# Performance work log

Hardware: AMD Instinct MI355X
Metric: run time of the kernel (lower is better)

## Reference

```python
import jax, jax.numpy as jnp
import numpy as np

N = 25000   # total nodes across the batch of graphs
K = 16      # sample_size_per_layer
H = 128     # encoder_hidden_dim
E = 128     # embedding_size
V = 32000   # vocab size
B = 50      # number of graphs / sql sequences
L = 128     # sql sequence length
NT = 4      # tokens per node name
NLAYERS = 3 # sample_layer_size


def _nrm(k, shape):
    return jax.random.normal(k, shape, dtype=jnp.float32) * 0.05


def setup_inputs() -> dict:
    key = jax.random.key(0)
    ks = iter(jax.random.split(key, 48))
    inp = {}
    inp["embed"] = _nrm(next(ks), (V, E))
    for d in ("seq_f", "seq_b", "node"):
        inp[d + "_Wih"] = _nrm(next(ks), (4 * H, E))
        inp[d + "_Whh"] = _nrm(next(ks), (4 * H, H))
        inp[d + "_b"] = _nrm(next(ks), (4 * H,))
    for d in ("fw", "bw"):
        inp[d + "_att0"] = _nrm(next(ks), (2, H))
        inp[d + "_attr"] = _nrm(next(ks), (NLAYERS - 1, 2, 2 * H))
        inp[d + "_Wg0"] = _nrm(next(ks), (H, H))
        inp[d + "_bg0"] = _nrm(next(ks), (H,))
        inp[d + "_Wgr"] = _nrm(next(ks), (NLAYERS - 1, 2 * H, 2 * H))
        inp[d + "_bgr"] = _nrm(next(ks), (NLAYERS - 1, 2 * H))
        inp[d + "_Wo0"] = _nrm(next(ks), (2, H, H))
        inp[d + "_bo0"] = _nrm(next(ks), (2, H))
        inp[d + "_Wor"] = _nrm(next(ks), (NLAYERS - 1, 2, 2 * H, H))
        inp[d + "_bor"] = _nrm(next(ks), (NLAYERS - 1, 2, H))
    inp["node_features"] = jax.random.randint(next(ks), (N, NT), 0, V)
    inp["fw_adj"] = jax.random.randint(next(ks), (N + 1, K), 0, N + 1)  # index N = zero-pad row
    inp["bw_adj"] = jax.random.randint(next(ks), (N + 1, K), 0, N + 1)
    inp["idx_sql_seqs"] = jax.random.randint(next(ks), (B, L), 0, V)
    lens = jax.random.randint(next(ks), (B,), 16, L + 1)
    inp["sql_seqs_lens"] = lens.at[0].set(L)  # ensure max(lens) == L like pad_packed
    inp["max_len"] = 1000  # nodes per graph (equal-size graphs)
    return inp


def _lstm(x, Wih, Whh, b):
    # x: [B, T, E] -> [B, T, H]; torch LSTM gate order i, f, g, o (bih+bhh folded into b)
    xg = jnp.einsum('bte,ge->btg', x, Wih) + b
    h0 = jnp.zeros((x.shape[0], Whh.shape[1]), x.dtype)
    def step(carry, gt):
        h, c = carry
        g = gt + h @ Whh.T
        i, f, gg, o = jnp.split(g, 4, axis=-1)
        c = jax.nn.sigmoid(f) * c + jax.nn.sigmoid(i) * jnp.tanh(gg)
        h = jax.nn.sigmoid(o) * jnp.tanh(c)
        return (h, c), h
    _, hs = jax.lax.scan(step, (h0, h0), jnp.swapaxes(xg, 0, 1))
    return jnp.swapaxes(hs, 0, 1)


def _gated_attn(self_h, neigh, att, Wg, bg, Wo, bo):
    # additive attention over K sampled neighbors, gated context, concat output (2*H)
    scores = jnp.einsum('nkd,d->nk', neigh, att[1]) + (self_h @ att[0])[:, None]
    a = jax.nn.softmax(scores, axis=-1)
    ctx = jnp.einsum('nk,nkd->nd', a, neigh)
    gate = jax.nn.sigmoid(self_h @ Wg + bg)
    from_self = jax.nn.relu(self_h @ Wo[0] + bo[0])
    from_neigh = jax.nn.relu((gate * ctx) @ Wo[1] + bo[1])
    return jnp.concatenate([from_self, from_neigh], axis=-1)


def reference(embed, seq_f_Wih, seq_f_Whh, seq_f_b, seq_b_Wih, seq_b_Whh, seq_b_b,
              node_Wih, node_Whh, node_b,
              fw_att0, fw_attr, fw_Wg0, fw_bg0, fw_Wgr, fw_bgr, fw_Wo0, fw_bo0, fw_Wor, fw_bor,
              bw_att0, bw_attr, bw_Wg0, bw_bg0, bw_Wgr, bw_bgr, bw_Wo0, bw_bo0, bw_Wor, bw_bor,
              node_features, fw_adj, bw_adj, idx_sql_seqs, sql_seqs_lens, max_len):
    Bq, Lq = idx_sql_seqs.shape
    # --- SQL sequence encoder: bi-LSTM with length-aware reverse (pack/pad semantics) ---
    se = embed[idx_sql_seqs]                              # [B, L, E]
    fwd = _lstm(se, seq_f_Wih, seq_f_Whh, seq_f_b)
    rev_idx = jnp.clip(sql_seqs_lens[:, None] - 1 - jnp.arange(Lq)[None, :], 0, Lq - 1)
    se_rev = jnp.take_along_axis(se, rev_idx[..., None], 1)
    bwd = jnp.take_along_axis(_lstm(se_rev, seq_b_Wih, seq_b_Whh, seq_b_b), rev_idx[..., None], 1)
    valid = (jnp.arange(Lq)[None, :] < sql_seqs_lens[:, None])[..., None]
    seqs_encoding = jnp.concatenate([fwd, bwd], -1) * valid  # padded positions zeroed
    seqs_encoding_mask = (idx_sql_seqs == 0)
    # --- node feature encoder: last hidden of a uni-LSTM over node tokens ---
    node_embedding = _lstm(embed[node_features], node_Wih, node_Whh, node_b)[:, -1, :]  # [N, H]
    fw_nbrs = fw_adj[:-1]  # [N, K]
    bw_nbrs = bw_adj[:-1]
    fw_hidden = node_embedding
    bw_hidden = node_embedding
    for l in range(NLAYERS):
        pad = jnp.zeros((1, fw_hidden.shape[1]), fw_hidden.dtype)
        fn = jnp.concatenate([fw_hidden, pad], 0)[fw_nbrs]  # [N, K, d]
        if l == 0:
            fw_hidden = _gated_attn(fw_hidden, fn, fw_att0, fw_Wg0, fw_bg0, fw_Wo0, fw_bo0)
        else:
            j = l - 1
            fw_hidden = _gated_attn(fw_hidden, fn, fw_attr[j], fw_Wgr[j], fw_bgr[j], fw_Wor[j], fw_bor[j])
        bn_ = jnp.concatenate([bw_hidden, pad], 0)[bw_nbrs]
        if l == 0:
            bw_hidden = _gated_attn(bw_hidden, bn_, bw_att0, bw_Wg0, bw_bg0, bw_Wo0, bw_bo0)
        else:
            j = l - 1
            bw_hidden = _gated_attn(bw_hidden, bn_, bw_attr[j], bw_Wgr[j], bw_bgr[j], bw_Wor[j], bw_bor[j])
    hidden = jax.nn.relu(jnp.concatenate([fw_hidden, bw_hidden], -1))  # [N, 4H]
    graph_hidden = hidden.reshape(hidden.shape[0] // max_len, max_len, hidden.shape[1])
    graph_embedding = graph_hidden.max(axis=1)
    return (graph_hidden, graph_embedding, max_len, seqs_encoding, seqs_encoding_mask)
```

## Files before the change

kernel.cpp:

```cpp
#include <hip/hip_runtime.h>
#include <math.h>

#define NN 25000
#define KNB 16
#define HH 128
#define VV 32000
#define BB 50
#define LL 128
#define NTK 4
#define NGRAPH 25
#define GCH 20

typedef __attribute__((ext_vector_type(8))) short s16x8;
typedef __attribute__((ext_vector_type(4))) float f32x4;
typedef _Float16 h16x2 __attribute__((ext_vector_type(2)));

__device__ __forceinline__ float fexp2(float x) {
#if __has_builtin(__builtin_amdgcn_exp2f)
    return __builtin_amdgcn_exp2f(x);
#else
    return exp2f(x);
#endif
}
__device__ __forceinline__ float frcp(float x) {
#if __has_builtin(__builtin_amdgcn_rcpf)
    return __builtin_amdgcn_rcpf(x);
#else
    return 1.f / x;
#endif
}
__device__ __forceinline__ float fsigm(float x) { return frcp(1.f + fexp2(x * -1.4426950408889634f)); }
__device__ __forceinline__ float ftanh(float x) { return 1.f - 2.f * frcp(1.f + fexp2(x * 2.8853900817779268f)); }

__device__ __forceinline__ unsigned short f2bf(float x) {
    unsigned int u = __float_as_uint(x);
    unsigned int r = (u + 0x7fffu + ((u >> 16) & 1u)) >> 16;
    return (unsigned short)r;
}
__device__ __forceinline__ float bf2f(unsigned int b) {
    return __uint_as_float((b & 0xffffu) << 16);
}

template<int CTRL>
__device__ __forceinline__ float qxor(float x) {
#if __has_builtin(__builtin_amdgcn_mov_dpp)
    return __int_as_float(__builtin_amdgcn_mov_dpp(__float_as_int(x), CTRL, 0xf, 0xf, true));
#else
    int m = (CTRL == 0xB1) ? 1 : (CTRL == 0x4E) ? 2 : 3;
    return __shfl_xor(x, m, 64);
#endif
}

__device__ __forceinline__ float hdot(unsigned int a, unsigned int b, float c) {
#if __has_builtin(__builtin_amdgcn_fdot2)
    return __builtin_amdgcn_fdot2(__builtin_bit_cast(h16x2, a), __builtin_bit_cast(h16x2, b), c, false);
#else
    h16x2 av = __builtin_bit_cast(h16x2, a), bv = __builtin_bit_cast(h16x2, b);
    return c + (float)av[0] * (float)bv[0] + (float)av[1] * (float)bv[1];
#endif
}

__global__ __launch_bounds__(256) void embconv_k(const float* __restrict__ e,
                                                 unsigned short* __restrict__ o)
{
    int i = blockIdx.x * 256 + threadIdx.x;
    if (i < VV * 128) o[i] = f2bf(e[i]);
}

__global__ __launch_bounds__(256) void wprep_k(
    const float* __restrict__ ndWih, const float* __restrict__ ndWhh,
    const float* __restrict__ fWg0, const float* __restrict__ fWgr,
    const float* __restrict__ fWo0, const float* __restrict__ fWor,
    const float* __restrict__ bWg0, const float* __restrict__ bWgr,
    const float* __restrict__ bWo0, const float* __restrict__ bWor,
    const float* __restrict__ sfWih, const float* __restrict__ sbWih,
    const float* __restrict__ sfWhh, const float* __restrict__ sbWhh,
    unsigned short* __restrict__ dst)
{
    int idx = blockIdx.x * 256 + threadIdx.x;
    if (idx >= 1146880) return;
    if (idx >= 884736) {
        int r = idx - 884736;
        int d = r >> 17;
        int o = r & 131071;
        int pairIdx = o >> 1, hf = o & 1;
        int k2 = pairIdx >> 9, n = pairIdx & 511;
        int k = k2 * 2 + hf;
        int unit = n >> 2, gate = n & 3;
        const float* W = d ? sbWhh : sfWhh;
        _Float16 hv = (_Float16)W[(gate * 128 + unit) * 128 + k];
        dst[idx] = __builtin_bit_cast(unsigned short, hv);
        return;
    }
    float val;
    if (idx < 131072) {
        int r = idx >> 8, k = idx & 255;
        int unit = r >> 2, gate = r & 3;
        int srow = (gate << 7) + unit;
        val = (k < 128) ? ndWih[srow * 128 + k] : ndWhh[srow * 128 + (k - 128)];
    } else if (idx < 753664) {
        int r = idx - 131072;
        int dir = r / 311296;
        int o = r % 311296;
        const float* Wg0 = dir ? bWg0 : fWg0;
        const float* Wgr = dir ? bWgr : fWgr;
        const float* Wo0 = dir ? bWo0 : fWo0;
        const float* Wor = dir ? bWor : fWor;
        if (o < 16384) {
            int n = o >> 7, k = o & 127;
            val = Wg0[k * 128 + n];
        } else if (o < 147456) {
            int p = o - 16384;
            int j = p >> 16, q = p & 65535;
            int n = q >> 8, k = q & 255;
            val = Wgr[j * 65536 + k * 256 + n];
        } else if (o < 180224) {
            int p = o - 147456;
            int s = p >> 14, q = p & 16383;
            int n = q >> 7, k = q & 127;
            val = Wo0[s * 16384 + k * 128 + n];
        } else {
            int p = o - 180224;
            int js = p >> 15, q = p & 32767;
            int n = q >> 8, k = q & 255;
            val = Wor[js * 32768 + k * 128 + n];
        }
    } else if (idx < 819200) {
        val = sfWih[idx - 753664];
    } else {
        val = sbWih[idx - 819200];
    }
    dst[idx] = f2bf(val);
}

__global__ __launch_bounds__(256) void tokrev_k(const int* __restrict__ idx,
                                                const int* __restrict__ lens,
                                                int* __restrict__ tokrev)
{
    int t = blockIdx.x * 256 + threadIdx.x;
    if (t >= BB * LL) return;
    int b = t / LL, tt = t % LL;
    int r = lens[b] - 1 - tt;
    r = r < 0 ? 0 : (r > LL - 1 ? LL - 1 : r);
    tokrev[t] = idx[b * LL + r];
}

__global__ __launch_bounds__(256) void hgemm1_k(
    const unsigned short* __restrict__ embedbf,
    const int* __restrict__ gidxA, const int* __restrict__ gidxB,
    const unsigned short* __restrict__ WtA, const unsigned short* __restrict__ WtB,
    const float* __restrict__ biasA, const float* __restrict__ biasB,
    float* __restrict__ outA, float* __restrict__ outB)
{
    __shared__ unsigned short Asm[128 * 64];
    __shared__ unsigned short Bsm[128 * 64];
    const int tid = threadIdx.x;
    const int lane = tid & 63, w = tid >> 6;
    const int wm = w >> 1, wn = w & 1;
    const int lane15 = lane & 15, hi = lane >> 4;
    const int y = blockIdx.y;
    const int* gidx = (y < 4) ? gidxA : gidxB;
    const unsigned short* Wt = (y < 4) ? WtA : WtB;
    const float* bias = (y < 4) ? biasA : biasB;
    float* outp = (y < 4) ? outA : outB;
    const int bm0 = blockIdx.x * 128, bn0 = (y & 3) * 128;
    const int M = BB * LL, K = 128;
    f32x4 acc[4][4];
#pragma unroll
    for (int i = 0; i < 4; ++i)
#pragma unroll
        for (int j = 0; j < 4; ++j) acc[i][j] = (f32x4){0.f, 0.f, 0.f, 0.f};

    for (int kt = 0; kt < K; kt += 64) {
#pragma unroll
        for (int r = 0; r < 4; ++r) {
            int id = tid + r * 256;
            int row = id >> 3, cc = id & 7;
            int m = bm0 + row;
            s16x8 v = {0, 0, 0, 0, 0, 0, 0, 0};
            if (m < M) {
                int g = gidx[m];
                v = *(const s16x8*)(embedbf + (size_t)g * 128 + kt + cc * 8);
            }
            int byt = (cc * 16) ^ ((row & 7) << 4);
            *(s16x8*)((char*)Asm + row * 128 + byt) = v;
        }
#pragma unroll
        for (int r = 0; r < 4; ++r) {
            int id = tid + r * 256;
            int row = id >> 3, cc = id & 7;
            s16x8 v = *(const s16x8*)(Wt + (size_t)(bn0 + row) * K + kt + cc * 8);
            int byt = (cc * 16) ^ ((row & 7) << 4);
            *(s16x8*)((char*)Bsm + row * 128 + byt) = v;
        }
        __syncthreads();
#pragma unroll
        for (int ks = 0; ks < 2; ++ks) {
            s16x8 af[4], bf[4];
#pragma unroll
            for (int mi = 0; mi < 4; ++mi) {
                int row = wm * 64 + mi * 16 + lane15;
                int byt = (ks * 64 + (hi * 16)) ^ ((row & 7) << 4);
                af[mi] = *(const s16x8*)((char*)Asm + row * 128 + byt);
            }
#pragma unroll
            for (int ni = 0; ni < 4; ++ni) {
                int row = wn * 64 + ni * 16 + lane15;
                int byt = (ks * 64 + (hi * 16)) ^ ((row & 7) << 4);
                bf[ni] = *(const s16x8*)((char*)Bsm + row * 128 + byt);
            }
#pragma unroll
            for (int mi = 0; mi < 4; ++mi)
#pragma unroll
                for (int ni = 0; ni < 4; ++ni)
                    acc[mi][ni] = __builtin_amdgcn_mfma_f32_16x16x32_bf16(af[mi], bf[ni], acc[mi][ni], 0, 0, 0);
        }
        __syncthreads();
    }
#pragma unroll
    for (int mi = 0; mi < 4; ++mi) {
#pragma unroll
        for (int ni = 0; ni < 4; ++ni) {
            int n = bn0 + wn * 64 + ni * 16 + lane15;
#pragma unroll
            for (int j = 0; j < 4; ++j) {
                int m = bm0 + wm * 64 + mi * 16 + hi * 4 + j;
                if (m < M) {
                    float v = acc[mi][ni][j] + bias[n];
                    int nn = ((n & 127) << 2) | (n >> 7);
                    outp[(size_t)m * 512 + nn] = v;
                }
            }
        }
    }
}

__global__ __launch_bounds__(512, 4) void node_seq_k(
    const unsigned short* __restrict__ embedbf,
    const int* __restrict__ nodefeat,
    const unsigned short* __restrict__ hrd,
    const unsigned short* __restrict__ nodeW,
    const float* __restrict__ ndb,
    unsigned short* __restrict__ hwr,
    unsigned short* __restrict__ cbuf,
    int step,
    const float* __restrict__ xgf, const float* __restrict__ xgb,
    const unsigned short* __restrict__ wseq,
    const int* __restrict__ lens,
    float* __restrict__ senc,
    unsigned short* __restrict__ hseq, float* __restrict__ cseq)
{
    __shared__ __align__(16) unsigned char smem[32768 + 512];
    const int bid = blockIdx.x;
    const int tid = threadIdx.x;

    if (bid >= 784) {
        int sid = bid - 784;
        int dir = sid >= BB ? 1 : 0;
        int b = dir ? sid - BB : sid;
        int len = lens[b];
        int t0 = step * 32;
        if (t0 >= len) return;
        int t1 = t0 + 32 < len ? t0 + 32 : len;
        const float* xg = (dir ? xgb : xgf) + (size_t)b * LL * 512;
        const unsigned int* wp = (const unsigned int*)(wseq + dir * 131072);
        int q = tid & 3, unit = tid >> 2;
        unsigned int wreg[64];
#pragma unroll
        for (int k2 = 0; k2 < 64; ++k2) wreg[k2] = wp[k2 * 512 + tid];
        unsigned short* hlsq = (unsigned short*)smem;
        float cj = 0.f;
        if (step == 0) {
            if (tid < 128) hlsq[tid] = 0;
        } else {
            if (tid < 128) hlsq[tid] = hseq[sid * 128 + tid];
            if (q == 0) cj = cseq[sid * 128 + unit];
        }
        __syncthreads();
        float xcur = xg[(size_t)t0 * 512 + tid];
        int pb = 0;
        for (int t = t0; t < t1; ++t) {
            float xnext = (t + 1 < t1) ? xg[(size_t)(t + 1) * 512 + tid] : 0.f;
            const uint4* hp = (const uint4*)&hlsq[pb * 128];
            float p0 = 0.f, p1 = 0.f, p2 = 0.f, p3 = 0.f;
#pragma unroll
            for (int i = 0; i < 4; ++i) {
                uint4 h0 = hp[i * 4 + 0], h1 = hp[i * 4 + 1], h2 = hp[i * 4 + 2], h3 = hp[i * 4 + 3];
                const unsigned int* w0 = &wreg[i * 16];
                p0 = hdot(h0.x, w0[0], p0);  p0 = hdot(h0.y, w0[1], p0);
                p0 = hdot(h0.z, w0[2], p0);  p0 = hdot(h0.w, w0[3], p0);
                p1 = hdot(h1.x, w0[4], p1);  p1 = hdot(h1.y, w0[5], p1);
                p1 = hdot(h1.z, w0[6], p1);  p1 = hdot(h1.w, w0[7], p1);
                p2 = hdot(h2.x, w0[8], p2);  p2 = hdot(h2.y, w0[9], p2);
                p2 = hdot(h2.z, w0[10], p2); p2 = hdot(h2.w, w0[11], p2);
                p3 = hdot(h3.x, w0[12], p3); p3 = hdot(h3.y, w0[13], p3);
                p3 = hdot(h3.z, w0[14], p3); p3 = hdot(h3.w, w0[15], p3);
            }
            float accv = xcur + ((p0 + p1) + (p2 + p3));
            float tv = (q == 2) ? ftanh(accv) : fsigm(accv);
            float v1 = __shfl_xor(tv, 1), v2 = __shfl_xor(tv, 2), v3 = __shfl_xor(tv, 3);
            if (q == 0) {
                cj = v1 * cj + tv * v2;
                float hv = v3 * ftanh(cj);
                _Float16 hh = (_Float16)hv;
                hlsq[(pb ^ 1) * 128 + unit] = __builtin_bit_cast(unsigned short, hh);
                int tout = dir ? (len - 1 - t) : t;
                senc[((size_t)b * LL + tout) * 256 + dir * 128 + unit] = hv;
            }
            __syncthreads();
            pb ^= 1;
            xcur = xnext;
        }
        if (q == 0) cseq[sid * 128 + unit] = cj;
        if (tid < 128) hseq[sid * 128 + tid] = hlsq[pb * 128 + tid];
        return;
    }

    unsigned short* Asm = (unsigned short*)smem;
    unsigned short* Bsm = (unsigned short*)(smem + 16384);
    const int lane = tid & 63, w = tid >> 6;
    const int wm = w & 1, wn = w >> 1;
    const int lane15 = lane & 15, hi = lane >> 4, q = lane & 3;
    const int bx = bid % 196, y = bid / 196;
    const int bm0 = bx * 128, bn0 = y * 128;
    const int czero = (step == 0);

    f32x4 acc[4][2];
#pragma unroll
    for (int i = 0; i < 4; ++i)
#pragma unroll
        for (int j = 0; j < 2; ++j) acc[i][j] = (f32x4){0.f, 0.f, 0.f, 0.f};

    for (int kt = 0; kt < 256; kt += 64) {
#pragma unroll
        for (int r = 0; r < 2; ++r) {
            int id = tid + r * 512;
            int row = id >> 3, cc = id & 7;
            int m = bm0 + row;
            s16x8 v = {0, 0, 0, 0, 0, 0, 0, 0};
            if (m < NN) {
                int k0 = kt + cc * 8;
                if (k0 < 128) {
                    int g = nodefeat[m * NTK + step];
                    v = *(const s16x8*)(embedbf + (size_t)g * 128 + k0);
                } else if (!czero) {
                    v = *(const s16x8*)(hrd + (size_t)m * 128 + (k0 - 128));
                }
            }
            int byt = (cc * 16) ^ ((row & 7) << 4);
            *(s16x8*)((char*)Asm + row * 128 + byt) = v;
        }
#pragma unroll
        for (int r = 0; r < 2; ++r) {
            int id = tid + r * 512;
            int row = id >> 3, cc = id & 7;
            s16x8 v = *(const s16x8*)(nodeW + (size_t)(bn0 + row) * 256 + kt + cc * 8);
            int byt = (cc * 16) ^ ((row & 7) << 4);
            *(s16x8*)((char*)Bsm + row * 128 + byt) = v;
        }
        __syncthreads();
#pragma unroll
        for (int ks = 0; ks < 2; ++ks) {
            s16x8 af[4], bf[2];
#pragma unroll
            for (int mi = 0; mi < 4; ++mi) {
                int row = wm * 64 + mi * 16 + lane15;
                int byt = (ks * 64 + (hi * 16)) ^ ((row & 7) << 4);
                af[mi] = *(const s16x8*)((char*)Asm + row * 128 + byt);
            }
#pragma unroll
            for (int ni = 0; ni < 2; ++ni) {
                int row = wn * 32 + ni * 16 + lane15;
                int byt = (ks * 64 + (hi * 16)) ^ ((row & 7) << 4);
                bf[ni] = *(const s16x8*)((char*)Bsm + row * 128 + byt);
            }
#pragma unroll
            for (int mi = 0; mi < 4; ++mi)
#pragma unroll
                for (int ni = 0; ni < 2; ++ni)
                    acc[mi][ni] = __builtin_amdgcn_mfma_f32_16x16x32_bf16(af[mi], bf[ni], acc[mi][ni], 0, 0, 0);
        }
        __syncthreads();
    }
    unsigned short* cb = cbuf + (((size_t)bid * 8 + w) * 64 + lane) * 8;
    float crv[8];
    if (czero) {
#pragma unroll
        for (int i = 0; i < 8; ++i) crv[i] = 0.f;
    } else {
        uint4 w0 = *(const uint4*)cb;
        unsigned int wd[4] = {w0.x, w0.y, w0.z, w0.w};
#pragma unroll
        for (int i = 0; i < 8; ++i) crv[i] = bf2f(wd[i >> 1] >> ((i & 1) * 16));
    }
    const bool qb0 = (lane & 1), qb1 = (lane & 2);
#pragma unroll
    for (int mi = 0; mi < 4; ++mi) {
#pragma unroll
        for (int ni = 0; ni < 2; ++ni) {
            int n = bn0 + wn * 32 + ni * 16 + lane15;
            int unit = n >> 2;
            float bval = ndb[((n & 3) << 7) + unit];
#pragma unroll
            for (int j = 0; j < 4; ++j) {
                float v = acc[mi][ni][j] + bval;
                float tv = (q == 2) ? ftanh(v) : fsigm(v);
                float v1 = qxor<0xB1>(tv), v2 = qxor<0x4E>(tv), v3 = qxor<0x1B>(tv);
                if (q == j) {
                    float gf = qb0 ? (qb1 ? v2 : tv) : (qb1 ? v3 : v1);
                    float gig = qb0 ? (v1 * v3) : (tv * v2);
                    float go = qb0 ? (qb1 ? tv : v2) : (qb1 ? v1 : v3);
                    float cc = gf * crv[mi * 2 + ni] + gig;
                    crv[mi * 2 + ni] = cc;
                    int m = bm0 + wm * 64 + mi * 16 + hi * 4 + j;
                    if (m < NN) hwr[(size_t)m * HH + unit] = f2bf(go * ftanh(cc));
                }
            }
        }
    }
    unsigned int wd[4];
#pragma unroll
    for (int p = 0; p < 4; ++p)
        wd[p] = (unsigned int)f2bf(crv[2 * p]) | ((unsigned int)f2bf(crv[2 * p + 1]) << 16);
    *(uint4*)cb = make_uint4(wd[0], wd[1], wd[2], wd[3]);
}

template<int D, int OF32OUT>
__global__ __launch_bounds__(512, 2) void layer_fused_k(
    const unsigned short* __restrict__ cur, int curds,
    const unsigned short* __restrict__ ctx, int ctxds,
    const unsigned short* __restrict__ wg, int wgds,
    const float* __restrict__ bgf, const float* __restrict__ bgb,
    const unsigned short* __restrict__ wo, int wods, int wrs,
    const float* __restrict__ bof, const float* __restrict__ bob,
    void* __restrict__ outb, int outds)
{
    __shared__ unsigned short As[64 * D];
    __shared__ unsigned short Gs[64 * D];
    __shared__ unsigned short Ws[128 * 64];
    constexpr int gt = D / 128;
    const int tid = threadIdx.x;
    const int lane = tid & 63, w = tid >> 6;
    const int wm = w >> 1, wn = w & 1;
    const int lane15 = lane & 15, hi = lane >> 4;
    const int orig = blockIdx.x;
    const int work = (orig & 7) * 98 + (orig >> 3);
    const int dir = work / 392;
    const int mt = work % 392;
    const int bm0 = mt * 64;
    const unsigned short* curd = cur + (size_t)dir * curds;
    const unsigned short* ctxd = ctx + (size_t)dir * ctxds;
    const float* bg = dir ? bgb : bgf;
    const float* bo = dir ? bob : bof;

    constexpr int CH = D / 8;
#pragma unroll
    for (int r = 0; r < D / 64; ++r) {
        int id = tid + r * 512;
        int row = id / CH, cc = id % CH;
        int m = bm0 + row;
        s16x8 v = {0, 0, 0, 0, 0, 0, 0, 0};
        if (m < NN) v = *(const s16x8*)(curd + (size_t)m * D + cc * 8);
        *(s16x8*)((char*)As + row * (D * 2) + ((cc * 16) ^ ((row & 7) << 4))) = v;
    }
    __syncthreads();

#pragma unroll
    for (int p = 0; p <= gt; ++p) {
        const bool isgate = p < gt;
        const int colBase = isgate ? p * 128 : 0;
        const unsigned short* Wt = isgate ? (wg + (size_t)dir * wgds + (size_t)colBase * D)
                                          : (wo + (size_t)dir * wods);
        f32x4 acc[4];
#pragma unroll
        for (int i = 0; i < 4; ++i) acc[i] = (f32x4){0.f, 0.f, 0.f, 0.f};
        for (int kt = 0; kt < D; kt += 64) {
#pragma unroll
            for (int r = 0; r < 2; ++r) {
                int id = tid + r * 512;
                int row = id >> 3, cc = id & 7;
                s16x8 v = *(const s16x8*)(Wt + (size_t)row * D + kt + cc * 8);
                *(s16x8*)((char*)Ws + row * 128 + ((cc * 16) ^ ((row & 7) << 4))) = v;
            }
            __syncthreads();
#pragma unroll
            for (int ks = 0; ks < 2; ++ks) {
                s16x8 af;
                {
                    int row = wm * 16 + lane15;
                    af = *(const s16x8*)((char*)As + row * (D * 2)
                              + (((kt + ks * 32 + hi * 8) * 2) ^ ((row & 7) << 4)));
                }
#pragma unroll
                for (int ni = 0; ni < 4; ++ni) {
                    int row = wn * 64 + ni * 16 + lane15;
                    s16x8 bf = *(const s16x8*)((char*)Ws + row * 128
                              + (((ks * 32 + hi * 8) * 2) ^ ((row & 7) << 4)));
                    acc[ni] = __builtin_amdgcn_mfma_f32_16x16x32_bf16(af, bf, acc[ni], 0, 0, 0);
                }
            }
            __syncthreads();
        }
#pragma unroll
        for (int ni = 0; ni < 4; ++ni) {
            int ncol = wn * 64 + ni * 16 + lane15;
#pragma unroll
            for (int j = 0; j < 4; ++j) {
                int rr = wm * 16 + hi * 4 + j;
                int m = bm0 + rr;
                if (isgate) {
                    int col = colBase + ncol;
                    float v = acc[ni][j] + bg[col];
                    int ma = (m < NN) ? m : 0;
                    v = fsigm(v) * bf2f(ctxd[(size_t)ma * D + col]);
                    unsigned int pv = f2bf(v);
                    unsigned int po = __shfl_xor((int)pv, 1);
                    if ((lane15 & 1) == 0) {
                        unsigned int word = pv | (po << 16);
                        *(unsigned int*)((char*)Gs + rr * (D * 2) + (((col * 2) & ~3) ^ ((rr & 7) << 4))) = word;
                    }
                } else if (m < NN) {
                    float v = fmaxf(acc[ni][j] + bo[ncol], 0.f);
                    if (OF32OUT) ((float*)outb)[(size_t)m * 512 + dir * 256 + ncol] = v;
                    else ((unsigned short*)outb)[(size_t)dir * outds + (size_t)m * 256 + ncol] = f2bf(v);
                }
            }
        }
    }
    __syncthreads();

    {
        const unsigned short* Wt = wo + (size_t)dir * wods + (size_t)wrs;
        f32x4 acc[4];
#pragma unroll
        for (int i = 0; i < 4; ++i) acc[i] = (f32x4){0.f, 0.f, 0.f, 0.f};
        for (int kt = 0; kt < D; kt += 64) {
#pragma unroll
            for (int r = 0; r < 2; ++r) {
                int id = tid + r * 512;
                int row = id >> 3, cc = id & 7;
                s16x8 v = *(const s16x8*)(Wt + (size_t)row * D + kt + cc * 8);
                *(s16x8*)((char*)Ws + row * 128 + ((cc * 16) ^ ((row & 7) << 4))) = v;
            }
            __syncthreads();
#pragma unroll
            for (int ks = 0; ks < 2; ++ks) {
                s16x8 af;
                {
                    int row = wm * 16 + lane15;
                    af = *(const s16x8*)((char*)Gs + row * (D * 2)
                              + (((kt + ks * 32 + hi * 8) * 2) ^ ((row & 7) << 4)));
                }
#pragma unroll
                for (int ni = 0; ni < 4; ++ni) {
                    int row = wn * 64 + ni * 16 + lane15;
                    s16x8 bf = *(const s16x8*)((char*)Ws + row * 128
                              + (((ks * 32 + hi * 8) * 2) ^ ((row & 7) << 4)));
                    acc[ni] = __builtin_amdgcn_mfma_f32_16x16x32_bf16(af, bf, acc[ni], 0, 0, 0);
                }
            }
            __syncthreads();
        }
#pragma unroll
        for (int ni = 0; ni < 4; ++ni) {
            int ncol = wn * 64 + ni * 16 + lane15;
#pragma unroll
            for (int j = 0; j < 4; ++j) {
                int m = bm0 + wm * 16 + hi * 4 + j;
                if (m < NN) {
                    float v = fmaxf(acc[ni][j] + bo[128 + ncol], 0.f);
                    if (OF32OUT) ((float*)outb)[(size_t)m * 512 + dir * 256 + 128 + ncol] = v;
                    else ((unsigned short*)outb)[(size_t)dir * outds + (size_t)m * 256 + 128 + ncol] = f2bf(v);
                }
            }
        }
    }
}

__global__ __launch_bounds__(256) void finalize_k(const int* __restrict__ idx,
                                                  const int* __restrict__ lens,
                                                  float* __restrict__ senc,
                                                  float* __restrict__ mask,
                                                  float* __restrict__ omax,
                                                  const int* __restrict__ mlin)
{
    int id = blockIdx.x * 256 + threadIdx.x;
    if (id == 0) omax[0] = (float)mlin[0];
    if (id >= BB * LL * 64) return;
    int row = id >> 6, c = id & 63;
    int b = row / LL, tt = row % LL;
    if (c == 0) mask[row] = (idx[row] == 0) ? 1.f : 0.f;
    if (tt >= lens[b]) *(float4*)&senc[(size_t)row * 256 + c * 4] = make_float4(0.f, 0.f, 0.f, 0.f);
}

template<int D>
__global__ __launch_bounds__(256) void sdot_k(const unsigned short* __restrict__ hidb, int hidds,
                                              const float* __restrict__ a1f, const float* __restrict__ a1b,
                                              float* __restrict__ s1)
{
    constexpr int V = D / 64;
    int dir = blockIdx.y;
    const unsigned short* hid = hidb + (size_t)dir * hidds;
    const float* att1 = dir ? a1b : a1f;
    int lane = threadIdx.x & 63, wid = threadIdx.x >> 6;
    int n = blockIdx.x * 4 + wid;
    if (n >= NN) return;
    float p = 0.f;
    if (V == 2) {
        unsigned int u = *(const unsigned int*)(hid + (size_t)n * D + lane * 2);
        p = bf2f(u) * att1[lane * 2] + bf2f(u >> 16) * att1[lane * 2 + 1];
    } else {
        uint2 u = *(const uint2*)(hid + (size_t)n * D + lane * 4);
        p = bf2f(u.x) * att1[lane * 4] + bf2f(u.x >> 16) * att1[lane * 4 + 1]
          + bf2f(u.y) * att1[lane * 4 + 2] + bf2f(u.y >> 16) * att1[lane * 4 + 3];
    }
#pragma unroll
    for (int m = 1; m < 64; m <<= 1) p += __shfl_xor(p, m);
    if (lane == 0) s1[dir * NN + n] = p;
}

template<int D>
__global__ __launch_bounds__(256) void attn_ctx3_k(const unsigned short* __restrict__ hidb, int hidds,
                                                   const int* __restrict__ adj0, const int* __restrict__ adj1,
                                                   const float* __restrict__ s1,
                                                   unsigned short* __restrict__ ctxb, int ctxds)
{
    constexpr int V = D / 64;
    int dir = blockIdx.y;
    const unsigned short* hid = hidb + (size_t)dir * hidds;
    const int* adj = dir ? adj1 : adj0;
    unsigned short* ctx = ctxb + (size_t)dir * ctxds;
    int lane = threadIdx.x & 63, wid = threadIdx.x >> 6;
    int n = blockIdx.x * 4 + wid;
    if (n >= NN) return;
    int nb[KNB];
    float sc[KNB];
#pragma unroll
    for (int k = 0; k < KNB; ++k) nb[k] = adj[n * KNB + k];
#pragma unroll
    for (int k = 0; k < KNB; ++k) sc[k] = (nb[k] < NN) ? s1[dir * NN + nb[k]] : 0.f;
    float mx = sc[0];
#pragma unroll
    for (int k = 1; k < KNB; ++k) mx = fmaxf(mx, sc[k]);
    float s = 0.f;
#pragma unroll
    for (int k = 0; k < KNB; ++k) { sc[k] = fexp2((sc[k] - mx) * 1.4426950408889634f); s += sc[k]; }
    float inv = frcp(s);
    float accv[V];
#pragma unroll
    for (int j = 0; j < V; ++j) accv[j] = 0.f;
#pragma unroll
    for (int k = 0; k < KNB; ++k) {
        if (nb[k] < NN) {
            if (V == 2) {
                unsigned int u = *(const unsigned int*)(hid + (size_t)nb[k] * D + lane * 2);
                accv[0] += sc[k] * bf2f(u);
                accv[1] += sc[k] * bf2f(u >> 16);
            } else {
                uint2 u = *(const uint2*)(hid + (size_t)nb[k] * D + lane * 4);
                accv[0] += sc[k] * bf2f(u.x);
                accv[1] += sc[k] * bf2f(u.x >> 16);
                accv[2] += sc[k] * bf2f(u.y);
                accv[3] += sc[k] * bf2f(u.y >> 16);
            }
        }
    }
#pragma unroll
    for (int j2 = 0; j2 < V; j2 += 2) {
        unsigned int pk = (unsigned int)f2bf(accv[j2] * inv) | ((unsigned int)f2bf(accv[j2 + 1] * inv) << 16);
        *(unsigned int*)(ctx + (size_t)n * D + lane * V + j2) = pk;
    }
}

__global__ __launch_bounds__(512) void gmax1_k(const float* __restrict__ gh, float* __restrict__ part)
{
    int g = blockIdx.x, ch = blockIdx.y;
    int c = threadIdx.x;
    const float* p = gh + ((size_t)g * 1000 + ch * (1000 / GCH)) * 512 + c;
    float m = -1e30f;
#pragma unroll 5
    for (int i = 0; i < 1000 / GCH; ++i) m = fmaxf(m, p[(size_t)i * 512]);
    part[((size_t)g * GCH + ch) * 512 + c] = m;
}

__global__ __launch_bounds__(512) void gmax2_k(const float* __restrict__ part, float* __restrict__ ge)
{
    int g = blockIdx.x;
    int c = threadIdx.x;
    float m = -1e30f;
#pragma unroll
    for (int i = 0; i < GCH; ++i) m = fmaxf(m, part[((size_t)g * GCH + i) * 512 + c]);
    ge[g * 512 + c] = m;
}

extern "C" void kernel_launch(void* const* d_in, const int* in_sizes, int n_in,
                              void* d_out, int out_size, void* d_ws, size_t ws_size,
                              hipStream_t stream)
{
    const float* embed = (const float*)d_in[0];
    const float* sfWhh = (const float*)d_in[2];
    const float* sfb   = (const float*)d_in[3];
    const float* sbWhh = (const float*)d_in[5];
    const float* sbb   = (const float*)d_in[6];
    const float* ndWih = (const float*)d_in[7];
    const float* ndWhh = (const float*)d_in[8];
    const float* ndb   = (const float*)d_in[9];
    const int* nodefeat = (const int*)d_in[30];
    const int* adj0     = (const int*)d_in[31];
    const int* adj1     = (const int*)d_in[32];
    const int* idxseq   = (const int*)d_in[33];
    const int* lens     = (const int*)d_in[34];
    const int* mlin     = (const int*)d_in[35];

    float* ws = (float*)d_ws;
    unsigned short* warena  = (unsigned short*)ws;
    unsigned short* embedbf = (unsigned short*)(ws + 573440);
    float* xgf = ws + 2621440;
    float* xgb = ws + 5898240;
    int*   tokrev = (int*)(ws + 9175040);
    unsigned short* hbf  = (unsigned short*)(ws + 9181440);
    unsigned short* hbf2 = (unsigned short*)(ws + 10781440);
    unsigned short* cbuf = (unsigned short*)(ws + 12381440);
    unsigned short* HA   = (unsigned short*)(ws + 573440);
    unsigned short* HB   = (unsigned short*)(ws + 6973440);
    unsigned short* ctxb = (unsigned short*)(ws + 13987072);
    float* s1buf = ws + 20387072;
    unsigned short* hseq = (unsigned short*)(ws + 20437072);
    float* cseq = ws + 20449872;
    float* gmaxp = ws + 573440;

    float* outf  = (float*)d_out;
    float* gh    = outf;
    float* ge    = outf + 12800000;
    float* omax  = outf + 12812800;
    float* senc  = outf + 12812801;
    float* omask = outf + 14451201;

    tokrev_k<<<dim3((BB * LL + 255) / 256), dim3(256), 0, stream>>>(idxseq, lens, tokrev);
    embconv_k<<<dim3(VV * 128 / 256), dim3(256), 0, stream>>>(embed, embedbf);
    wprep_k<<<dim3(4480), dim3(256), 0, stream>>>(ndWih, ndWhh,
        (const float*)d_in[12], (const float*)d_in[14], (const float*)d_in[16], (const float*)d_in[18],
        (const float*)d_in[22], (const float*)d_in[24], (const float*)d_in[26], (const float*)d_in[28],
        (const float*)d_in[1], (const float*)d_in[4], sfWhh, sbWhh, warena);

    hgemm1_k<<<dim3(50, 8), dim3(256), 0, stream>>>(embedbf, idxseq, tokrev,
        warena + 753664, warena + 819200, sfb, sbb, xgf, xgb);

    for (int t = 0; t < NTK; ++t) {
        const unsigned short* hrd = (t & 1) ? hbf2 : hbf;
        unsigned short* hwr = (t & 1) ? hbf : hbf2;
        node_seq_k<<<dim3(884), dim3(512), 0, stream>>>(embedbf, nodefeat, hrd,
            warena, ndb, hwr, cbuf, t,
            xgf, xgb, warena + 884736, lens, senc, hseq, cseq);
    }
    finalize_k<<<dim3(1600), dim3(256), 0, stream>>>(idxseq, lens, senc, omask, omax, mlin);

    for (int l = 0; l < 3; ++l) {
        int D = (l == 0) ? 128 : 256;
        int j = l - 1;
        const unsigned short* curb = (l == 0) ? hbf : (l == 1 ? HA : HB);
        int curds = (l == 0) ? 0 : NN * 256;
        int ctxds = NN * D;
        const float* a1f = (l == 0) ? (const float*)d_in[10] + 128 : (const float*)d_in[11] + (size_t)j * 512 + 256;
        const float* a1b = (l == 0) ? (const float*)d_in[20] + 128 : (const float*)d_in[21] + (size_t)j * 512 + 256;

        if (D == 128) {
            sdot_k<128><<<dim3(NN / 4, 2), dim3(256), 0, stream>>>(curb, curds, a1f, a1b, s1buf);
            attn_ctx3_k<128><<<dim3(NN / 4, 2), dim3(256), 0, stream>>>(curb, curds, adj0, adj1, s1buf, ctxb, ctxds);
        } else {
            sdot_k<256><<<dim3(NN / 4, 2), dim3(256), 0, stream>>>(curb, curds, a1f, a1b, s1buf);
            attn_ctx3_k<256><<<dim3(NN / 4, 2), dim3(256), 0, stream>>>(curb, curds, adj0, adj1, s1buf, ctxb, ctxds);
        }

        const unsigned short* wgb = warena + 131072 + ((l == 0) ? 0 : 16384 + j * 65536);
        const float* bgf = (l == 0) ? (const float*)d_in[13] : (const float*)d_in[15] + (size_t)j * 256;
        const float* bgb = (l == 0) ? (const float*)d_in[23] : (const float*)d_in[25] + (size_t)j * 256;
        const unsigned short* wob = warena + 131072 + ((l == 0) ? 147456 : 180224 + j * 65536);
        int wrs = (l == 0) ? 16384 : 32768;
        const float* bof = (l == 0) ? (const float*)d_in[17] : (const float*)d_in[19] + (size_t)j * 256;
        const float* bob = (l == 0) ? (const float*)d_in[27] : (const float*)d_in[29] + (size_t)j * 256;
        int outds = NN * 256;

        if (l == 0) {
            layer_fused_k<128, 0><<<dim3(784), dim3(512), 0, stream>>>(curb, curds, ctxb, ctxds,
                wgb, 311296, bgf, bgb, wob, 311296, wrs, bof, bob, HA, outds);
        } else if (l == 1) {
            layer_fused_k<256, 0><<<dim3(784), dim3(512), 0, stream>>>(curb, curds, ctxb, ctxds,
                wgb, 311296, bgf, bgb, wob, 311296, wrs, bof, bob, HB, outds);
        } else {
            layer_fused_k<256, 1><<<dim3(784), dim3(512), 0, stream>>>(curb, curds, ctxb, ctxds,
                wgb, 311296, bgf, bgb, wob, 311296, wrs, bof, bob, gh, 0);
        }
    }

    gmax1_k<<<dim3(NGRAPH, GCH), dim3(512), 0, stream>>>(gh, gmaxp);
    gmax2_k<<<dim3(NGRAPH), dim3(512), 0, stream>>>(gmaxp, ge);
}
```

Baseline: 563.9 us.

## Fuse neighbor attention context aggregation into the layer GEMM kernel

Removes the separate attention-context kernel and computes the softmax-weighted neighbor aggregation inside layer_fused_k, storing it in shared memory (Gs) and reading it there in the gate epilogue. The sdot kernel now emits exp(score) directly, so the max-subtraction in the softmax is dropped. This saves a global write and re-read of the context tensor plus one launch per layer. The cost is more work per GEMM block before the MFMA stage, and without the max shift large scores could overflow. Pad neighbors now get weight 1 in the softmax denominator instead of the exp(0-max) the old code used.

Measured after the change: 714.0 us. 26.6% more time.

```diff
diff --git a/kernel.cpp b/kernel.cpp
--- a/kernel.cpp
+++ b/kernel.cpp
@@ -428,7 +428,8 @@
 template<int D, int OF32OUT>
 __global__ __launch_bounds__(512, 2) void layer_fused_k(
     const unsigned short* __restrict__ cur, int curds,
-    const unsigned short* __restrict__ ctx, int ctxds,
+    const int* __restrict__ adj0, const int* __restrict__ adj1,
+    const float* __restrict__ es1,
     const unsigned short* __restrict__ wg, int wgds,
     const float* __restrict__ bgf, const float* __restrict__ bgb,
     const unsigned short* __restrict__ wo, int wods, int wrs,
@@ -439,6 +440,7 @@
     __shared__ unsigned short Gs[64 * D];
     __shared__ unsigned short Ws[128 * 64];
     constexpr int gt = D / 128;
+    constexpr int V = D / 64;
     const int tid = threadIdx.x;
     const int lane = tid & 63, w = tid >> 6;
     const int wm = w >> 1, wn = w & 1;
@@ -449,9 +451,58 @@
     const int mt = work % 392;
     const int bm0 = mt * 64;
     const unsigned short* curd = cur + (size_t)dir * curds;
-    const unsigned short* ctxd = ctx + (size_t)dir * ctxds;
     const float* bg = dir ? bgb : bgf;
     const float* bo = dir ? bob : bof;
+
+    {
+        const int* adj = dir ? adj1 : adj0;
+        const float* es1d = es1 + dir * NN;
+#pragma unroll
+        for (int i = 0; i < 8; ++i) {
+            int rr = w * 8 + i;
+            int n = bm0 + rr;
+            float accv[V];
+#pragma unroll
+            for (int j = 0; j < V; ++j) accv[j] = 0.f;
+            float inv = 0.f;
+            if (n < NN) {
+                int nb[KNB];
+                float sc[KNB];
+#pragma unroll
+                for (int k = 0; k < KNB; ++k) nb[k] = adj[n * KNB + k];
+                float s = 0.f;
+#pragma unroll
+                for (int k = 0; k < KNB; ++k) { sc[k] = (nb[k] < NN) ? es1d[nb[k]] : 1.f; s += sc[k]; }
+                inv = frcp(s);
+#pragma unroll
+                for (int k = 0; k < KNB; ++k) {
+                    if (nb[k] < NN) {
+                        if (V == 2) {
+                            unsigned int u = *(const unsigned int*)(curd + (size_t)nb[k] * D + lane * 2);
+                            accv[0] += sc[k] * bf2f(u);
+                            accv[1] += sc[k] * bf2f(u >> 16);
+                        } else {
+                            uint2 u = *(const uint2*)(curd + (size_t)nb[k] * D + lane * 4);
+                            accv[0] += sc[k] * bf2f(u.x);
+                            accv[1] += sc[k] * bf2f(u.x >> 16);
+                            accv[2] += sc[k] * bf2f(u.y);
+                            accv[3] += sc[k] * bf2f(u.y >> 16);
+                        }
+                    }
+                }
+            }
+            if (V == 2) {
+                unsigned int pk = (unsigned int)f2bf(accv[0] * inv) | ((unsigned int)f2bf(accv[1] * inv) << 16);
+                int byt = ((lane * 4)) ^ ((rr & 7) << 4);
+                *(unsigned int*)((char*)Gs + rr * (D * 2) + byt) = pk;
+            } else {
+                unsigned int p0 = (unsigned int)f2bf(accv[0] * inv) | ((unsigned int)f2bf(accv[1] * inv) << 16);
+                unsigned int p1 = (unsigned int)f2bf(accv[2] * inv) | ((unsigned int)f2bf(accv[3] * inv) << 16);
+                int byt = ((lane * 8)) ^ ((rr & 7) << 4);
+                *(uint2*)((char*)Gs + rr * (D * 2) + byt) = make_uint2(p0, p1);
+            }
+        }
+    }
 
     constexpr int CH = D / 8;
 #pragma unroll
@@ -511,8 +562,9 @@
                 if (isgate) {
                     int col = colBase + ncol;
                     float v = acc[ni][j] + bg[col];
-                    int ma = (m < NN) ? m : 0;
-                    v = fsigm(v) * bf2f(ctxd[(size_t)ma * D + col]);
+                    float cv = bf2f(*(const unsigned short*)((char*)Gs + rr * (D * 2)
+                                    + ((col * 2) ^ ((rr & 7) << 4))));
+                    v = fsigm(v) * cv;
                     unsigned int pv = f2bf(v);
                     unsigned int po = __shfl_xor((int)pv, 1);
                     if ((lane15 & 1) == 0) {
@@ -616,60 +668,7 @@
     }
 #pragma unroll
     for (int m = 1; m < 64; m <<= 1) p += __shfl_xor(p, m);
-    if (lane == 0) s1[dir * NN + n] = p;
-}
-
-template<int D>
-__global__ __launch_bounds__(256) void attn_ctx3_k(const unsigned short* __restrict__ hidb, int hidds,
-                                                   const int* __restrict__ adj0, const int* __restrict__ adj1,
-                                                   const float* __restrict__ s1,
-                                                   unsigned short* __restrict__ ctxb, int ctxds)
-{
-    constexpr int V = D / 64;
-    int dir = blockIdx.y;
-    const unsigned short* hid = hidb + (size_t)dir * hidds;
-    const int* adj = dir ? adj1 : adj0;
-    unsigned short* ctx = ctxb + (size_t)dir * ctxds;
-    int lane = threadIdx.x & 63, wid = threadIdx.x >> 6;
-    int n = blockIdx.x * 4 + wid;
-    if (n >= NN) return;
-    int nb[KNB];
-    float sc[KNB];
-#pragma unroll
-    for (int k = 0; k < KNB; ++k) nb[k] = adj[n * KNB + k];
-#pragma unroll
-    for (int k = 0; k < KNB; ++k) sc[k] = (nb[k] < NN) ? s1[dir * NN + nb[k]] : 0.f;
-    float mx = sc[0];
-#pragma unroll
-    for (int k = 1; k < KNB; ++k) mx = fmaxf(mx, sc[k]);
-    float s = 0.f;
-#pragma unroll
-    for (int k = 0; k < KNB; ++k) { sc[k] = fexp2((sc[k] - mx) * 1.4426950408889634f); s += sc[k]; }
-    float inv = frcp(s);
-    float accv[V];
-#pragma unroll
-    for (int j = 0; j < V; ++j) accv[j] = 0.f;
-#pragma unroll
-    for (int k = 0; k < KNB; ++k) {
-        if (nb[k] < NN) {
-            if (V == 2) {
-                unsigned int u = *(const unsigned int*)(hid + (size_t)nb[k] * D + lane * 2);
-                accv[0] += sc[k] * bf2f(u);
-                accv[1] += sc[k] * bf2f(u >> 16);
-            } else {
-                uint2 u = *(const uint2*)(hid + (size_t)nb[k] * D + lane * 4);
-                accv[0] += sc[k] * bf2f(u.x);
-                accv[1] += sc[k] * bf2f(u.x >> 16);
-                accv[2] += sc[k] * bf2f(u.y);
-                accv[3] += sc[k] * bf2f(u.y >> 16);
-            }
-        }
-    }
-#pragma unroll
-    for (int j2 = 0; j2 < V; j2 += 2) {
-        unsigned int pk = (unsigned int)f2bf(accv[j2] * inv) | ((unsigned int)f2bf(accv[j2 + 1] * inv) << 16);
-        *(unsigned int*)(ctx + (size_t)n * D + lane * V + j2) = pk;
-    }
+    if (lane == 0) s1[dir * NN + n] = fexp2(p * 1.4426950408889634f);
 }
 
 __global__ __launch_bounds__(512) void gmax1_k(const float* __restrict__ gh, float* __restrict__ part)
@@ -723,11 +722,10 @@
     unsigned short* cbuf = (unsigned short*)(ws + 12381440);
     unsigned short* HA   = (unsigned short*)(ws + 573440);
     unsigned short* HB   = (unsigned short*)(ws + 6973440);
-    unsigned short* ctxb = (unsigned short*)(ws + 13987072);
     float* s1buf = ws + 20387072;
     unsigned short* hseq = (unsigned short*)(ws + 20437072);
     float* cseq = ws + 20449872;
-    float* gmaxp = ws + 573440;
+    float* gmaxp = ws + 13987072;
 
     float* outf  = (float*)d_out;
     float* gh    = outf;
@@ -760,17 +758,13 @@
         int j = l - 1;
         const unsigned short* curb = (l == 0) ? hbf : (l == 1 ? HA : HB);
         int curds = (l == 0) ? 0 : NN * 256;
-        int ctxds = NN * D;
         const float* a1f = (l == 0) ? (const float*)d_in[10] + 128 : (const float*)d_in[11] + (size_t)j * 512 + 256;
         const float* a1b = (l == 0) ? (const float*)d_in[20] + 128 : (const float*)d_in[21] + (size_t)j * 512 + 256;
 
-        if (D == 128) {
+        if (D == 128)
             sdot_k<128><<<dim3(NN / 4, 2), dim3(256), 0, stream>>>(curb, curds, a1f, a1b, s1buf);
-            attn_ctx3_k<128><<<dim3(NN / 4, 2), dim3(256), 0, stream>>>(curb, curds, adj0, adj1, s1buf, ctxb, ctxds);
-        } else {
+        else
             sdot_k<256><<<dim3(NN / 4, 2), dim3(256), 0, stream>>>(curb, curds, a1f, a1b, s1buf);
-            attn_ctx3_k<256><<<dim3(NN / 4, 2), dim3(256), 0, stream>>>(curb, curds, adj0, adj1, s1buf, ctxb, ctxds);
-        }
 
         const unsigned short* wgb = warena + 131072 + ((l == 0) ? 0 : 16384 + j * 65536);
         const float* bgf = (l == 0) ? (const float*)d_in[13] : (const float*)d_in[15] + (size_t)j * 256;
@@ -782,13 +776,13 @@
         int outds = NN * 256;
 
         if (l == 0) {
-            layer_fused_k<128, 0><<<dim3(784), dim3(512), 0, stream>>>(curb, curds, ctxb, ctxds,
+            layer_fused_k<128, 0><<<dim3(784), dim3(512), 0, stream>>>(curb, curds, adj0, adj1, s1buf,
                 wgb, 311296, bgf, bgb, wob, 311296, wrs, bof, bob, HA, outds);
         } else if (l == 1) {
-            layer_fused_k<256, 0><<<dim3(784), dim3(512), 0, stream>>>(curb, curds, ctxb, ctxds,
+            layer_fused_k<256, 0><<<dim3(784), dim3(512), 0, stream>>>(curb, curds, adj0, adj1, s1buf,
                 wgb, 311296, bgf, bgb, wob, 311296, wrs, bof, bob, HB, outds);
         } else {
-            layer_fused_k<256, 1><<<dim3(784), dim3(512), 0, stream>>>(curb, curds, ctxb, ctxds,
+            layer_fused_k<256, 1><<<dim3(784), dim3(512), 0, stream>>>(curb, curds, adj0, adj1, s1buf,
                 wgb, 311296, bgf, bgb, wob, 311296, wrs, bof, bob, gh, 0);
         }
     }
```
